# Performance work log

Measured on AMD Instinct MI355X. Metric: run time of the kernel, lower is better.

Reference implementation:

```python
import jax, jax.numpy as jnp
import numpy as np

K = 1024
T = 16384
P = 2          # number of lags
N_STAGES = 2   # len(s_list)
EDGE_P = 0.005 # edge density -> avg degree ~5


def setup_inputs() -> dict:
    key = jax.random.key(0)
    kX, kA, ka, kb0, kb1 = jax.random.split(key, 5)
    X = jax.random.normal(kX, (K, T), dtype=jnp.float32)
    # sparse symmetric 0/1 adjacency, zero diagonal
    U = jax.random.uniform(kA, (K, K))
    Ab = (U < EDGE_P)
    Ab = (Ab | Ab.T) & ~jnp.eye(K, dtype=bool)
    A = Ab.astype(jnp.float32)
    alpha = jax.random.normal(ka, (P,), dtype=jnp.float32)
    beta0 = jax.random.normal(kb0, (P,), dtype=jnp.float32)
    beta1 = jax.random.normal(kb1, (P,), dtype=jnp.float32)
    return {"X": X, "A": A, "alpha": alpha, "beta0": beta0, "beta1": beta1}


def _stage_avg_matrices(A):
    """M[r] averages over nodes at shortest-path distance exactly r+1 (rows with
    no stage-r neighbors are all-zero, matching the `if neighbors:` guard)."""
    Ab = A > 0.5
    Af = Ab.astype(jnp.float32)
    reach_prev = jnp.eye(A.shape[0], dtype=bool)  # distance <= 0
    Ms = []
    for _ in range(N_STAGES):
        reach = reach_prev | ((reach_prev.astype(jnp.float32) @ Af) > 0.5)
        exact = reach & ~reach_prev                     # distance == r+1
        exact_f = exact.astype(jnp.float32)
        deg = exact_f.sum(axis=1, keepdims=True)        # (K, 1)
        M = exact_f / jnp.maximum(deg, 1.0)             # zero rows stay zero
        Ms.append(M)
        reach_prev = reach
    return Ms


def reference(X, A, alpha, beta0, beta1):
    K_, T_ = X.shape
    betas = [beta0, beta1]
    Ms = _stage_avg_matrices(A)
    # one dense aggregation per stage over ALL time steps, then slice lags
    MXs = [M @ X for M in Ms]                           # each (K, T)
    Y = jnp.zeros((K_, T_ - P), dtype=X.dtype)
    for lag in range(1, P + 1):
        sl = slice(P - lag, T_ - lag)
        Y = Y + alpha[lag - 1] * X[:, sl]
        for stage in range(N_STAGES):
            Y = Y + betas[stage][lag - 1] * MXs[stage][:, sl]
    return Y
```

## Files before the change

### kernel.cpp

```cpp
#include <hip/hip_runtime.h>

typedef float fx4 __attribute__((ext_vector_type(4)));
typedef short s16x8 __attribute__((ext_vector_type(8)));
typedef __bf16 bfx8 __attribute__((ext_vector_type(8)));

#define KN 1024
#define TT 16384
#define NOUT 16382
#define NKT 32
#define COLP 16640
#define HLDS 49664

#define APK_OFF 34078720u
#define B1_OFF  (APK_OFF + 4194304u)

__device__ __forceinline__ unsigned short f2bf(float f) {
  return __builtin_bit_cast(unsigned short, (__bf16)f);
}

__device__ __forceinline__ void gll16(const void* g, void* l) {
  __builtin_amdgcn_global_load_lds(
      (const __attribute__((address_space(1))) void*)g,
      (__attribute__((address_space(3))) void*)l, 16, 0, 0);
}

__global__ __launch_bounds__(256) void k_masks(const float* __restrict__ A,
                                               unsigned* __restrict__ B1) {
  int k = blockIdx.x;
  int tid = threadIdx.x;
  int wv = tid >> 6, lane = tid & 63;
  for (int i = 0; i < 4; ++i) {
    int n = i * 256 + wv * 64 + lane;
    bool bit = (A[(size_t)k * KN + n] > 0.5f) && (n != k);
    unsigned long long m = __ballot(bit);
    if (lane == 0) {
      B1[k * 32 + i * 8 + wv * 2]     = (unsigned)m;
      B1[k * 32 + i * 8 + wv * 2 + 1] = (unsigned)(m >> 32);
    }
  }
}

__global__ __launch_bounds__(256) void k_wp(const unsigned* __restrict__ B1,
                                            const float* __restrict__ alpha,
                                            const float* __restrict__ beta0,
                                            const float* __restrict__ beta1,
                                            const float* __restrict__ X,
                                            unsigned short* __restrict__ Wc,
                                            unsigned short* __restrict__ Xbf) {
  int tid = threadIdx.x;
  if (blockIdx.x >= 1024) {
    int p = blockIdx.x - 1024;
    int o = p & 127;
    int cb = p >> 7;
    int c = cb * 256 + tid;
    unsigned v[4];
#pragma unroll
    for (int q = 0; q < 4; ++q) {
      float f0 = 0.f, f1 = 0.f;
      if (c < TT) {
        f0 = X[(size_t)(o * 8 + q * 2) * TT + c];
        f1 = X[(size_t)(o * 8 + q * 2 + 1) * TT + c];
      }
      v[q] = (unsigned)f2bf(f0) | ((unsigned)f2bf(f1) << 16);
    }
    uint4 w; w.x = v[0]; w.y = v[1]; w.z = v[2]; w.w = v[3];
    *reinterpret_cast<uint4*>(Xbf + ((size_t)o * COLP + c) * 8) = w;
    return;
  }
  __shared__ unsigned reach[32];
  __shared__ unsigned ex2[32];
  __shared__ unsigned short list[1056];
  __shared__ int nl;
  int k = blockIdx.x;
  if (tid == 0) nl = 0;
  if (tid < 32) {
    unsigned r = B1[k * 32 + tid];
    if (tid == (k >> 5)) r |= 1u << (k & 31);
    reach[tid] = r;
    ex2[tid] = 0;
  }
  __syncthreads();
  for (int m = tid; m < KN; m += 256)
    if ((reach[m >> 5] >> (m & 31)) & 1) {
      int i = atomicAdd(&nl, 1);
      list[i] = (unsigned short)m;
    }
  __syncthreads();
  int n2 = nl;
  for (int i = 0; i < n2; ++i) {
    int m = list[i];
    if (tid < 32) ex2[tid] |= B1[m * 32 + tid];
  }
  __syncthreads();
  if (tid < 32) ex2[tid] &= ~reach[tid];
  __syncthreads();
  int d1 = 0, d2 = 0;
  for (int w = 0; w < 32; ++w) { d1 += __popc(reach[w]); d2 += __popc(ex2[w]); }
  d1 -= 1;
  float rd1 = 1.0f / fmaxf((float)d1, 1.0f);
  float rd2 = 1.0f / fmaxf((float)d2, 1.0f);
  float c00 = beta0[0] * rd1, c01 = beta0[1] * rd1;
  float c10 = beta1[0] * rd2, c11 = beta1[1] * rd2;
  float a0 = alpha[0], a1 = alpha[1];
  int mb = k >> 8, rloc = k & 255;
  for (int q = 0; q < 4; ++q) {
    int n = tid * 4 + q;
    bool in1 = (((reach[n >> 5] >> (n & 31)) & 1) != 0) && (n != k);
    bool in2 = ((ex2[n >> 5] >> (n & 31)) & 1) != 0;
    float v0 = (in1 ? c00 : 0.f) + (in2 ? c10 : 0.f) + (n == k ? a0 : 0.f);
    float v1 = (in1 ? c01 : 0.f) + (in2 ? c11 : 0.f) + (n == k ? a1 : 0.f);
    int t = n >> 5, kb2 = (n >> 3) & 3, ii = n & 7;
    size_t base = (size_t)mb * 524288 +
                  ((((size_t)t * 2) * 4 + kb2) * 256 + rloc) * 8 + ii;
    Wc[base] = f2bf(v0);
    Wc[base + 8192] = f2bf(v1);
  }
}

__global__ __launch_bounds__(512, 2) void k_gemm(const char* __restrict__ Apk,
                                                 const char* __restrict__ Xbf,
                                                 float* __restrict__ Y) {
  __shared__ __align__(16) char lds[3 * HLDS];
  int bid = blockIdx.x;
  int swz = (bid & 7) * 32 + (bid >> 3);
  int jb = swz >> 2, mb = swz & 3;
  int tid = threadIdx.x;
  int lane = tid & 63, wv = tid >> 6;
  int wm = wv >> 2, wn = wv & 3;
  int kb = lane >> 4, ml = lane & 15;
  const char* Asrc = Apk + (size_t)mb * 1048576;

  fx4 acc[2][4][4];
#pragma unroll
  for (int q = 0; q < 2; ++q)
#pragma unroll
    for (int a = 0; a < 4; ++a)
#pragma unroll
      for (int b = 0; b < 4; ++b) acc[q][a][b] = (fx4){0.f, 0.f, 0.f, 0.f};

  auto stageA = [&](int buf, int ts, int s) {
    char* dst = lds + buf * HLDS + s * 16384;
    const char* src = Asrc + ((size_t)ts * 2 + s) * 16384;
    gll16(src + tid * 16, dst + tid * 16);
    gll16(src + tid * 16 + 8192, dst + tid * 16 + 8192);
  };
  auto stageB = [&](int buf, int ts) {
    char* dstB = lds + buf * HLDS + 32768;
#pragma unroll
    for (int u2 = 0; u2 < 2; ++u2) {
      int u = tid + u2 * 512;
      int kbq = u >> 8, cu = u & 255;
      const char* src = Xbf + ((size_t)(ts * 4 + kbq) * COLP + jb * 256 + cu) * 16;
      gll16(src, dstB + (kbq * 264 + cu) * 16);
    }
    if ((tid & 127) == 0) {
      int kbq = tid >> 7;
      uint4 v = *reinterpret_cast<const uint4*>(
          Xbf + ((size_t)(ts * 4 + kbq) * COLP + jb * 256 + 256) * 16);
      *reinterpret_cast<uint4*>(dstB + (kbq * 264 + 256) * 16) = v;
    }
  };

#define READ_A(dst, buf, s, qm)                                                     \
  do {                                                                              \
    const char* Ah_ = lds + (buf) * HLDS + (s) * 16384;                             \
    _Pragma("unroll") for (int mf = 0; mf < 4; ++mf)                                \
      dst[mf] = *(const s16x8*)(Ah_ +                                               \
          (size_t)(kb * 256 + wm * 128 + (qm) * 64 + mf * 16 + ml) * 16);           \
  } while (0)
#define READ_B(dst, buf, off)                                                       \
  do {                                                                              \
    const char* Bh_ = lds + (buf) * HLDS + 32768;                                   \
    _Pragma("unroll") for (int nf = 0; nf < 4; ++nf)                                \
      dst[nf] = *(const s16x8*)(Bh_ +                                               \
          (size_t)(kb * 264 + wn * 64 + nf * 16 + ml + (off)) * 16);                \
  } while (0)
#define MFMA16(acc_, a_, b_)                                                        \
  do {                                                                              \
    __builtin_amdgcn_s_setprio(1);                                                  \
    _Pragma("unroll") for (int mf = 0; mf < 4; ++mf)                                \
      _Pragma("unroll") for (int nf = 0; nf < 4; ++nf)                              \
        acc_[mf][nf] = __builtin_amdgcn_mfma_f32_16x16x32_bf16(                     \
            __builtin_bit_cast(bfx8, a_[mf]), __builtin_bit_cast(bfx8, b_[nf]),     \
            acc_[mf][nf], 0, 0, 0);                                                 \
    __builtin_amdgcn_s_setprio(0);                                                  \
  } while (0)

  s16x8 aA[4], aB[4], bU[4], bV[4];

  stageA(0, 0, 0); stageA(0, 0, 1); stageB(0, 0);
  stageA(1, 1, 0); stageA(1, 1, 1); stageB(1, 1);
  asm volatile("s_waitcnt vmcnt(6)" ::: "memory");
  asm volatile("s_waitcnt lgkmcnt(0)" ::: "memory");
  __builtin_amdgcn_s_barrier();

  int bR = 0, bW = 2;
  for (int kt = 0; kt < NKT; ++kt) {
    int ts2 = (kt + 2) & (NKT - 1);
    READ_B(bU, bR, 1);
    READ_A(aA, bR, 0, 0);
    stageA(bW, ts2, 0);
    MFMA16(acc[0], aA, bU);
    READ_A(aB, bR, 0, 1);
    stageA(bW, ts2, 1);
    MFMA16(acc[1], aB, bU);
    READ_B(bV, bR, 0);
    READ_A(aA, bR, 1, 0);
    stageB(bW, ts2);
    MFMA16(acc[0], aA, bV);
    READ_A(aB, bR, 1, 1);
    MFMA16(acc[1], aB, bV);
    asm volatile("s_waitcnt vmcnt(6)" ::: "memory");
    asm volatile("s_waitcnt lgkmcnt(0)" ::: "memory");
    __builtin_amdgcn_s_barrier();
    bR = (bR == 2) ? 0 : bR + 1;
    bW = (bW == 2) ? 0 : bW + 1;
  }
  asm volatile("s_waitcnt vmcnt(0)" ::: "memory");

  int c0 = jb * 256 + wn * 64;
  int r0 = mb * 256 + wm * 128;
#pragma unroll
  for (int qm = 0; qm < 2; ++qm)
#pragma unroll
    for (int mf = 0; mf < 4; ++mf)
#pragma unroll
      for (int nf = 0; nf < 4; ++nf) {
        int c = c0 + nf * 16 + ml;
        if (c < NOUT) {
          int r = r0 + qm * 64 + mf * 16 + (lane >> 4) * 4;
#pragma unroll
          for (int i = 0; i < 4; ++i)
            Y[(size_t)(r + i) * NOUT + c] = acc[qm][mf][nf][i];
        }
      }
#undef READ_A
#undef READ_B
#undef MFMA16
}

extern "C" void kernel_launch(void* const* d_in, const int* in_sizes, int n_in,
                              void* d_out, int out_size, void* d_ws, size_t ws_size,
                              hipStream_t stream) {
  const float* X     = (const float*)d_in[0];
  const float* A     = (const float*)d_in[1];
  const float* alpha = (const float*)d_in[2];
  const float* beta0 = (const float*)d_in[3];
  const float* beta1 = (const float*)d_in[4];
  float* Y = (float*)d_out;
  char* ws = (char*)d_ws;
  char* Xbf = ws;
  char* Apk = ws + APK_OFF;
  unsigned* B1 = (unsigned*)(ws + B1_OFF);

  k_masks<<<dim3(1024), dim3(256), 0, stream>>>(A, B1);
  k_wp<<<dim3(9344), dim3(256), 0, stream>>>(B1, alpha, beta0, beta1, X,
                                             (unsigned short*)Apk,
                                             (unsigned short*)Xbf);
  k_gemm<<<dim3(256), dim3(512), 0, stream>>>(Apk, Xbf, Y);
}
```

Baseline: 92.79 us.

## Switch GEMM to double-buffered LDS with staggered wave-group pass order

Replaces the triple-buffered LDS pipeline with two buffers, cutting per-block LDS from about 149KB to about 98KB. Wave groups alternate the order of their two shift passes so their LDS reads are staggered. The B tile layout drops the row padding and places the extra halo column in a separate slot. The aim is to lower LDS footprint and simplify the waits, at the cost of a shallower prefetch depth (full vmcnt(0) wait every iteration), which may expose global load latency.

```diff
diff --git a/kernel.cpp b/kernel.cpp
--- a/kernel.cpp
+++ b/kernel.cpp
@@ -9,7 +9,7 @@
 #define NOUT 16382
 #define NKT 32
 #define COLP 16640
-#define HLDS 49664
+#define HLDS 49216
 
 #define APK_OFF 34078720u
 #define B1_OFF  (APK_OFF + 4194304u)
@@ -110,8 +110,8 @@
     float v0 = (in1 ? c00 : 0.f) + (in2 ? c10 : 0.f) + (n == k ? a0 : 0.f);
     float v1 = (in1 ? c01 : 0.f) + (in2 ? c11 : 0.f) + (n == k ? a1 : 0.f);
     int t = n >> 5, kb2 = (n >> 3) & 3, ii = n & 7;
-    size_t base = (size_t)mb * 524288 +
-                  ((((size_t)t * 2) * 4 + kb2) * 256 + rloc) * 8 + ii;
+    size_t base = (size_t)mb * 524288 + (size_t)t * 16384 +
+                  kb2 * 2048 + rloc * 8 + ii;
     Wc[base] = f2bf(v0);
     Wc[base + 8192] = f2bf(v1);
   }
@@ -120,13 +120,14 @@
 __global__ __launch_bounds__(512, 2) void k_gemm(const char* __restrict__ Apk,
                                                  const char* __restrict__ Xbf,
                                                  float* __restrict__ Y) {
-  __shared__ __align__(16) char lds[3 * HLDS];
+  __shared__ __align__(16) char lds[2 * HLDS];
   int bid = blockIdx.x;
   int swz = (bid & 7) * 32 + (bid >> 3);
   int jb = swz >> 2, mb = swz & 3;
   int tid = threadIdx.x;
   int lane = tid & 63, wv = tid >> 6;
   int wm = wv >> 2, wn = wv & 3;
+  int fl = (wv >> 2) & 1;
   int kb = lane >> 4, ml = lane & 15;
   const char* Asrc = Apk + (size_t)mb * 1048576;
 
@@ -138,42 +139,48 @@
 #pragma unroll
       for (int b = 0; b < 4; ++b) acc[q][a][b] = (fx4){0.f, 0.f, 0.f, 0.f};
 
-  auto stageA = [&](int buf, int ts, int s) {
-    char* dst = lds + buf * HLDS + s * 16384;
-    const char* src = Asrc + ((size_t)ts * 2 + s) * 16384;
-    gll16(src + tid * 16, dst + tid * 16);
-    gll16(src + tid * 16 + 8192, dst + tid * 16 + 8192);
+  auto stageA = [&](int t) {
+    char* dst = lds + (t & 1) * HLDS;
+    const char* src = Asrc + (size_t)(t & (NKT - 1)) * 32768;
+#pragma unroll
+    for (int u = 0; u < 4; ++u)
+      gll16(src + tid * 16 + u * 8192, dst + tid * 16 + u * 8192);
   };
-  auto stageB = [&](int buf, int ts) {
-    char* dstB = lds + buf * HLDS + 32768;
+  auto stageB = [&](int t) {
+    char* dstB = lds + (t & 1) * HLDS + 32768;
+    int ts = t & (NKT - 1);
 #pragma unroll
     for (int u2 = 0; u2 < 2; ++u2) {
       int u = tid + u2 * 512;
-      int kbq = u >> 8, cu = u & 255;
-      const char* src = Xbf + ((size_t)(ts * 4 + kbq) * COLP + jb * 256 + cu) * 16;
-      gll16(src, dstB + (kbq * 264 + cu) * 16);
-    }
-    if ((tid & 127) == 0) {
-      int kbq = tid >> 7;
-      uint4 v = *reinterpret_cast<const uint4*>(
-          Xbf + ((size_t)(ts * 4 + kbq) * COLP + jb * 256 + 256) * 16);
-      *reinterpret_cast<uint4*>(dstB + (kbq * 264 + 256) * 16) = v;
+      const char* src = Xbf +
+          ((size_t)(ts * 4 + (u >> 8)) * COLP + jb * 256 + (u & 255)) * 16;
+      gll16(src, dstB + u * 16);
+    }
+    if (tid < 4) {
+      const char* src = Xbf +
+          ((size_t)(ts * 4 + tid) * COLP + jb * 256 + 256) * 16;
+      gll16(src, dstB + 16384);
     }
   };
 
-#define READ_A(dst, buf, s, qm)                                                     \
-  do {                                                                              \
-    const char* Ah_ = lds + (buf) * HLDS + (s) * 16384;                             \
+#define READ_A(dst, t, s, qm)                                                       \
+  do {                                                                              \
+    const char* Ah_ = lds + ((t) & 1) * HLDS + (s) * 16384;                         \
     _Pragma("unroll") for (int mf = 0; mf < 4; ++mf)                                \
       dst[mf] = *(const s16x8*)(Ah_ +                                               \
           (size_t)(kb * 256 + wm * 128 + (qm) * 64 + mf * 16 + ml) * 16);           \
   } while (0)
-#define READ_B(dst, buf, off)                                                       \
-  do {                                                                              \
-    const char* Bh_ = lds + (buf) * HLDS + 32768;                                   \
-    _Pragma("unroll") for (int nf = 0; nf < 4; ++nf)                                \
-      dst[nf] = *(const s16x8*)(Bh_ +                                               \
-          (size_t)(kb * 264 + wn * 64 + nf * 16 + ml + (off)) * 16);                \
+#define READ_B(dst, t, off)                                                         \
+  do {                                                                              \
+    const char* Bh_ = lds + ((t) & 1) * HLDS + 32768;                               \
+    _Pragma("unroll") for (int nf = 0; nf < 4; ++nf) {                              \
+      int c_ = wn * 64 + nf * 16 + ml + (off);                                      \
+      const char* a_ = Bh_ + (size_t)(kb * 256 + c_) * 16;                          \
+      if ((off) == 1 && nf == 3) {                                                  \
+        if (c_ == 256) a_ = Bh_ + 16384 + kb * 16;                                  \
+      }                                                                             \
+      dst[nf] = *(const s16x8*)a_;                                                  \
+    }                                                                               \
   } while (0)
 #define MFMA16(acc_, a_, b_)                                                        \
   do {                                                                              \
@@ -186,37 +193,34 @@
     __builtin_amdgcn_s_setprio(0);                                                  \
   } while (0)
 
-  s16x8 aA[4], aB[4], bU[4], bV[4];
-
-  stageA(0, 0, 0); stageA(0, 0, 1); stageB(0, 0);
-  stageA(1, 1, 0); stageA(1, 1, 1); stageB(1, 1);
-  asm volatile("s_waitcnt vmcnt(6)" ::: "memory");
-  asm volatile("s_waitcnt lgkmcnt(0)" ::: "memory");
+#define S_PASS(s, DO_STAGE)                                                         \
+  do {                                                                              \
+    READ_B(bA, kt, 1 - (s));                                                        \
+    READ_A(aA, kt, s, 0);                                                           \
+    if (DO_STAGE) stageA(kt + 1);                                                   \
+    MFMA16(acc[0], aA, bA);                                                         \
+    READ_A(aB, kt, s, 1);                                                           \
+    if (DO_STAGE) stageB(kt + 1);                                                   \
+    MFMA16(acc[1], aB, bA);                                                         \
+  } while (0)
+
+  s16x8 aA[4], aB[4], bA[4];
+
+  stageA(0); stageB(0);
+  asm volatile("s_waitcnt vmcnt(0)" ::: "memory");
   __builtin_amdgcn_s_barrier();
 
-  int bR = 0, bW = 2;
   for (int kt = 0; kt < NKT; ++kt) {
-    int ts2 = (kt + 2) & (NKT - 1);
-    READ_B(bU, bR, 1);
-    READ_A(aA, bR, 0, 0);
-    stageA(bW, ts2, 0);
-    MFMA16(acc[0], aA, bU);
-    READ_A(aB, bR, 0, 1);
-    stageA(bW, ts2, 1);
-    MFMA16(acc[1], aB, bU);
-    READ_B(bV, bR, 0);
-    READ_A(aA, bR, 1, 0);
-    stageB(bW, ts2);
-    MFMA16(acc[0], aA, bV);
-    READ_A(aB, bR, 1, 1);
-    MFMA16(acc[1], aB, bV);
-    asm volatile("s_waitcnt vmcnt(6)" ::: "memory");
-    asm volatile("s_waitcnt lgkmcnt(0)" ::: "memory");
+    if (fl == 0) {
+      S_PASS(0, 1);
+      S_PASS(1, 0);
+    } else {
+      S_PASS(1, 1);
+      S_PASS(0, 0);
+    }
+    asm volatile("s_waitcnt vmcnt(0)" ::: "memory");
     __builtin_amdgcn_s_barrier();
-    bR = (bR == 2) ? 0 : bR + 1;
-    bW = (bW == 2) ? 0 : bW + 1;
-  }
-  asm volatile("s_waitcnt vmcnt(0)" ::: "memory");
+  }
 
   int c0 = jb * 256 + wn * 64;
   int r0 = mb * 256 + wm * 128;
@@ -237,6 +241,7 @@
 #undef READ_A
 #undef READ_B
 #undef MFMA16
+#undef S_PASS
 }
 
 extern "C" void kernel_launch(void* const* d_in, const int* in_sizes, int n_in,
```

Result: faster. 83.96 us (-9.5%).
